# Kernel tuning notes

Measured on AMD Instinct MI355X. Metric: run time of the kernel, lower is better.

## Reference

```python
import jax, jax.numpy as jnp
import numpy as np

BETA = 0.25  # commitment weight (legacy=False)


def setup_inputs() -> dict:
    key = jax.random.key(0)
    k1, k2 = jax.random.split(key)
    B, N_E, E_DIM = 32768, 8192, 256
    z = jax.random.normal(k1, (B, E_DIM), dtype=jnp.float32)
    # embedding initialized uniform(-1/n_e, 1/n_e) as in the torch module
    emb_weight = jax.random.uniform(k2, (N_E, E_DIM), dtype=jnp.float32,
                                    minval=-1.0 / N_E, maxval=1.0 / N_E)
    return {"z": z, "emb_weight": emb_weight}


def reference(z, emb_weight):
    # pairwise squared distances: ||z||^2 + ||e||^2 - 2 z.e   -> [B, n_e]
    d = (jnp.sum(z * z, axis=1, keepdims=True)
         + jnp.sum(emb_weight * emb_weight, axis=1)
         - 2.0 * jnp.einsum('bd,nd->bn', z, emb_weight))
    idx = jnp.argmin(d, axis=1)            # [B]
    z_q = emb_weight[idx]                  # [B, e_dim] gather
    sg = jax.lax.stop_gradient
    loss = (BETA * jnp.mean((sg(z_q) - z) ** 2)
            + jnp.mean((z_q - sg(z)) ** 2))
    z_q_st = z + sg(z_q - z)               # straight-through estimator
    return (z_q_st, loss)
```

## Files before the change

### kernel.cpp

```cpp
#include <hip/hip_runtime.h>
#include <hip/hip_bf16.h>


#define B_ROWS 32768
#define N_E    8192
#define E_DIM  256
#define NSPLIT 4
#define NB     32
#define TILE_B (NB * 256)
#define NBUF   4
#define NIT    ((N_E / NSPLIT) / NB)
#define IDXMASK 0xFFFFE000u

typedef __attribute__((ext_vector_type(4)))  float f32x4;
typedef __attribute__((ext_vector_type(16))) float f32x16;
typedef __attribute__((ext_vector_type(4)))  int   i32x4;
typedef __attribute__((ext_vector_type(8)))  int   i32x8;

#define WAIT_BAR(N) asm volatile("s_waitcnt vmcnt(" #N ")\n\ts_barrier" ::: "memory")

__global__ void cast_e_kernel(const float* __restrict__ emb,
                              int* __restrict__ eb8) {
    int row  = (blockIdx.x * blockDim.x + threadIdx.x) >> 6;
    int lane = threadIdx.x & 63;
    if (row >= N_E) return;
    const float4 v = ((const float4*)(emb + (size_t)row * E_DIM))[lane];
    const float s = 8192.0f;
    int r = __builtin_amdgcn_cvt_pk_fp8_f32(v.x * s, v.y * s, 0, false);
    r     = __builtin_amdgcn_cvt_pk_fp8_f32(v.z * s, v.w * s, r, true);
    eb8[(size_t)row * 64 + lane] = r;
}

__device__ __forceinline__ void stage_tile(char* buf, const char* ebB,
                                           int n0, int wv, int lane) {
    #pragma unroll
    for (int r = 0; r < 2; ++r) {
        const int addr = r * 4096 + (wv * 64 + lane) * 16;
        const int e  = addr >> 8;
        const int Xs = addr & 255;
        const int o  = Xs ^ ((e & 15) << 4);
        const char* src = ebB + ((size_t)(n0 + e) << 8) + o;
        __builtin_amdgcn_global_load_lds((const void*)src,
                                         (void*)(buf + addr), 16, 0, 0);
    }
}

__global__ __launch_bounds__(256, 2) void vq_main_kernel(
        const float* __restrict__ z,
        const int* __restrict__ eb8,
        float* __restrict__ bval) {
    __shared__ __align__(16) char lds[NBUF][TILE_B];
    char* lds0 = &lds[0][0];
    const int tid  = threadIdx.x;
    const int lane = tid & 63;
    const int wv   = tid >> 6;
    const int e    = lane & 31;
    const int hi   = lane >> 5;
    const int rowblk = (int)blockIdx.x >> 2;
    const int split  = (int)blockIdx.x & 3;
    const int rowbase = rowblk * 256 + wv * 64;
    const int n_begin = split * (N_E / NSPLIT);
    const char* ebB = (const char*)eb8;

    i32x8 a[2][4];
    #pragma unroll
    for (int s = 0; s < 2; ++s) {
        const float* zr = z + (size_t)(rowbase + s * 32 + e) * E_DIM + hi * 32;
        #pragma unroll
        for (int c = 0; c < 4; ++c) {
            const float4* p = (const float4*)(zr + c * 64);
            i32x8 f;
            #pragma unroll
            for (int q = 0; q < 8; ++q) {
                const float4 v = p[q];
                int r = __builtin_amdgcn_cvt_pk_fp8_f32(v.x, v.y, 0, false);
                r     = __builtin_amdgcn_cvt_pk_fp8_f32(v.z, v.w, r, true);
                f[q] = r;
            }
            a[s][c] = f;
        }
    }

    int boff[8];
    #pragma unroll
    for (int i = 0; i < 8; ++i) {
        const int X = (i >> 1) * 64 + hi * 32 + (i & 1) * 16;
        boff[i] = e * 256 + (X ^ ((e & 15) << 4));
    }

    float rmax[2][16];
    #pragma unroll
    for (int s = 0; s < 2; ++s)
        #pragma unroll
        for (int r = 0; r < 16; ++r) rmax[s][r] = -__builtin_huge_valf();

    unsigned ibase = (unsigned)(n_begin + e);

    auto compute = [&](int t) {
        const char* cbuf = lds0 + (t & (NBUF - 1)) * TILE_B;
        i32x8 b[4];
        #pragma unroll
        for (int c = 0; c < 4; ++c) {
            const i32x4 lo = *(const i32x4*)(cbuf + boff[c * 2]);
            const i32x4 hi4 = *(const i32x4*)(cbuf + boff[c * 2 + 1]);
            b[c][0] = lo[0]; b[c][1] = lo[1]; b[c][2] = lo[2]; b[c][3] = lo[3];
            b[c][4] = hi4[0]; b[c][5] = hi4[1]; b[c][6] = hi4[2]; b[c][7] = hi4[3];
        }
        f32x16 acc0 = {0.f,0.f,0.f,0.f,0.f,0.f,0.f,0.f,
                       0.f,0.f,0.f,0.f,0.f,0.f,0.f,0.f};
        f32x16 acc1 = acc0;
        __builtin_amdgcn_s_setprio(1);
        #pragma unroll
        for (int c = 0; c < 4; ++c) {
            acc0 = __builtin_amdgcn_mfma_scale_f32_32x32x64_f8f6f4(
                a[0][c], b[c], acc0, 0, 0, 0, 127, 0, 127);
            acc1 = __builtin_amdgcn_mfma_scale_f32_32x32x64_f8f6f4(
                a[1][c], b[c], acc1, 0, 0, 0, 127, 0, 127);
        }
        __builtin_amdgcn_s_setprio(0);
        #pragma unroll
        for (int r = 0; r < 16; ++r) {
            unsigned p0 = (__builtin_bit_cast(unsigned, acc0[r]) & IDXMASK) | ibase;
            rmax[0][r] = fmaxf(rmax[0][r], __builtin_bit_cast(float, p0));
            unsigned p1 = (__builtin_bit_cast(unsigned, acc1[r]) & IDXMASK) | ibase;
            rmax[1][r] = fmaxf(rmax[1][r], __builtin_bit_cast(float, p1));
        }
        ibase += NB;
    };

    stage_tile(lds0 + 0 * TILE_B, ebB, n_begin + 0 * NB, wv, lane);
    stage_tile(lds0 + 1 * TILE_B, ebB, n_begin + 1 * NB, wv, lane);
    stage_tile(lds0 + 2 * TILE_B, ebB, n_begin + 2 * NB, wv, lane);

    #pragma unroll 1
    for (int t = 0; t < NIT - 2; ++t) {
        WAIT_BAR(4);
        if (t < NIT - 3)
            stage_tile(lds0 + ((t + 3) & (NBUF - 1)) * TILE_B, ebB,
                       n_begin + (t + 3) * NB, wv, lane);
        compute(t);
    }
    WAIT_BAR(2);
    compute(NIT - 2);
    WAIT_BAR(0);
    compute(NIT - 1);

    #pragma unroll
    for (int s = 0; s < 2; ++s) {
        #pragma unroll
        for (int r = 0; r < 16; ++r) {
            float v = rmax[s][r];
            #pragma unroll
            for (int bit = 1; bit < 32; bit <<= 1)
                v = fmaxf(v, __shfl_xor(v, bit));
            if (e == 0) {
                const int row = rowbase + s * 32 + (r & 3) + 8 * (r >> 2) + 4 * hi;
                bval[(size_t)split * B_ROWS + row] = v;
            }
        }
    }
}

__global__ void gather_kernel(const float* __restrict__ z,
                              const float* __restrict__ emb,
                              const float* __restrict__ bval,
                              float* __restrict__ out,
                              float* __restrict__ partials) {
    __shared__ float sred[4];
    const int lane   = threadIdx.x & 63;
    const int waveid = threadIdx.x >> 6;
    const int row    = blockIdx.x * 4 + waveid;

    float bv = bval[row];
    #pragma unroll
    for (int s = 1; s < NSPLIT; ++s)
        bv = fmaxf(bv, bval[(size_t)s * B_ROWS + row]);
    const int idx = (int)(__builtin_bit_cast(unsigned, bv) & 0x1FFFu);

    const float4 e  = ((const float4*)(emb + (size_t)idx * E_DIM))[lane];
    const float4 zz = ((const float4*)(z + (size_t)row * E_DIM))[lane];
    ((float4*)(out + (size_t)row * E_DIM))[lane] = e;

    float dx = e.x - zz.x, dy = e.y - zz.y, dz = e.z - zz.z, dw = e.w - zz.w;
    float s = dx * dx + dy * dy + dz * dz + dw * dw;
    #pragma unroll
    for (int off = 32; off; off >>= 1) s += __shfl_xor(s, off);
    if (lane == 0) sred[waveid] = s;
    __syncthreads();
    if (threadIdx.x == 0)
        partials[blockIdx.x] = (sred[0] + sred[1]) + (sred[2] + sred[3]);
}

__global__ void loss_kernel(const float* __restrict__ partials,
                            float* __restrict__ out) {
    __shared__ float sm[256];
    float s = 0.f;
    for (int i = threadIdx.x; i < B_ROWS / 4; i += 256) s += partials[i];
    sm[threadIdx.x] = s;
    __syncthreads();
    for (int off = 128; off; off >>= 1) {
        if (threadIdx.x < off) sm[threadIdx.x] += sm[threadIdx.x + off];
        __syncthreads();
    }
    if (threadIdx.x == 0)
        out[(size_t)B_ROWS * E_DIM] = 1.25f * sm[0] / (float)((size_t)B_ROWS * E_DIM);
}

extern "C" void kernel_launch(void* const* d_in, const int* in_sizes, int n_in,
                              void* d_out, int out_size, void* d_ws, size_t ws_size,
                              hipStream_t stream) {
    const float* z   = (const float*)d_in[0];
    const float* emb = (const float*)d_in[1];
    float* out = (float*)d_out;

    char* ws = (char*)d_ws;
    int*    eb8      = (int*)ws;
    float*  bval     = (float*)(ws + (2u << 20));
    float*  partials = (float*)(ws + (2u << 20) + (512u << 10));

    hipLaunchKernelGGL(cast_e_kernel, dim3(N_E / 4), dim3(256), 0, stream, emb, eb8);
    hipLaunchKernelGGL(vq_main_kernel, dim3(128 * NSPLIT), dim3(256), 0, stream, z, eb8, bval);
    hipLaunchKernelGGL(gather_kernel, dim3(B_ROWS / 4), dim3(256), 0, stream, z, emb, bval, out, partials);
    hipLaunchKernelGGL(loss_kernel, dim3(1), dim3(256), 0, stream, partials, out);
}
```

Baseline: 103.1 us.

## Double-buffer LDS codebook fragments in registers to overlap reads with MFMA

Splits the per-tile work into an LDS-to-register load step and an MFMA/argmax step. The main loop is unrolled by two with ping-pong register buffers, so the next tile's fragments are read from LDS while the current tile's MFMAs run. The global-to-LDS prefetch schedule and wait counts are adjusted to match, with a new epilogue. This hides LDS read latency behind matrix work, at the cost of about 32 extra VGPRs per lane and more complex wait and barrier ordering.

```diff
diff --git a/kernel.cpp b/kernel.cpp
--- a/kernel.cpp
+++ b/kernel.cpp
@@ -96,16 +96,17 @@
 
     unsigned ibase = (unsigned)(n_begin + e);
 
-    auto compute = [&](int t) {
+    auto load_b = [&](i32x8* dst, int t) {
         const char* cbuf = lds0 + (t & (NBUF - 1)) * TILE_B;
-        i32x8 b[4];
         #pragma unroll
         for (int c = 0; c < 4; ++c) {
-            const i32x4 lo = *(const i32x4*)(cbuf + boff[c * 2]);
+            const i32x4 lo  = *(const i32x4*)(cbuf + boff[c * 2]);
             const i32x4 hi4 = *(const i32x4*)(cbuf + boff[c * 2 + 1]);
-            b[c][0] = lo[0]; b[c][1] = lo[1]; b[c][2] = lo[2]; b[c][3] = lo[3];
-            b[c][4] = hi4[0]; b[c][5] = hi4[1]; b[c][6] = hi4[2]; b[c][7] = hi4[3];
-        }
+            dst[c] = __builtin_shufflevector(lo, hi4, 0, 1, 2, 3, 4, 5, 6, 7);
+        }
+    };
+
+    auto mfma_pack = [&](const i32x8* b) {
         f32x16 acc0 = {0.f,0.f,0.f,0.f,0.f,0.f,0.f,0.f,
                        0.f,0.f,0.f,0.f,0.f,0.f,0.f,0.f};
         f32x16 acc1 = acc0;
@@ -128,22 +129,39 @@
         ibase += NB;
     };
 
+    i32x8 bA[4], bB[4];
+
     stage_tile(lds0 + 0 * TILE_B, ebB, n_begin + 0 * NB, wv, lane);
     stage_tile(lds0 + 1 * TILE_B, ebB, n_begin + 1 * NB, wv, lane);
     stage_tile(lds0 + 2 * TILE_B, ebB, n_begin + 2 * NB, wv, lane);
+    WAIT_BAR(4);
+    load_b(bA, 0);
 
     #pragma unroll 1
-    for (int t = 0; t < NIT - 2; ++t) {
-        WAIT_BAR(4);
-        if (t < NIT - 3)
-            stage_tile(lds0 + ((t + 3) & (NBUF - 1)) * TILE_B, ebB,
-                       n_begin + (t + 3) * NB, wv, lane);
-        compute(t);
+    for (int t = 0; t < NIT - 4; t += 2) {
+        WAIT_BAR(2);
+        stage_tile(lds0 + ((t + 3) & (NBUF - 1)) * TILE_B, ebB,
+                   n_begin + (t + 3) * NB, wv, lane);
+        load_b(bB, t + 1);
+        mfma_pack(bA);
+        WAIT_BAR(2);
+        stage_tile(lds0 + ((t + 4) & (NBUF - 1)) * TILE_B, ebB,
+                   n_begin + (t + 4) * NB, wv, lane);
+        load_b(bA, t + 2);
+        mfma_pack(bB);
     }
     WAIT_BAR(2);
-    compute(NIT - 2);
+    stage_tile(lds0 + ((NIT - 1) & (NBUF - 1)) * TILE_B, ebB,
+               n_begin + (NIT - 1) * NB, wv, lane);
+    load_b(bB, NIT - 3);
+    mfma_pack(bA);
+    WAIT_BAR(2);
+    load_b(bA, NIT - 2);
+    mfma_pack(bB);
     WAIT_BAR(0);
-    compute(NIT - 1);
+    load_b(bB, NIT - 1);
+    mfma_pack(bA);
+    mfma_pack(bB);
 
     #pragma unroll
     for (int s = 0; s < 2; ++s) {
```

Measured after the change: 103.4 us. About the same (+0.3%).

## Replace LDS-staged codebook tiles with direct per-wave register double-buffered loads

Applied to the files above, without the earlier changes.

Removes the shared-memory staging of FP8 codebook tiles (global_load_lds with a 4-deep ring and barriers). Each single-wave block now loads its B fragments straight from global memory into registers, double-buffered with ping-pong arrays. The grid changes from 256-thread blocks to 64-thread blocks, so there are four times as many blocks. This drops barrier and LDS overhead, but codebook data is no longer shared across waves, so global/L2 traffic for the codebook goes up about fourfold and load latency is less hidden.

```diff
diff --git a/kernel.cpp b/kernel.cpp
--- a/kernel.cpp
+++ b/kernel.cpp
@@ -7,8 +7,6 @@
 #define E_DIM  256
 #define NSPLIT 4
 #define NB     32
-#define TILE_B (NB * 256)
-#define NBUF   4
 #define NIT    ((N_E / NSPLIT) / NB)
 #define IDXMASK 0xFFFFE000u
 
@@ -16,8 +14,6 @@
 typedef __attribute__((ext_vector_type(16))) float f32x16;
 typedef __attribute__((ext_vector_type(4)))  int   i32x4;
 typedef __attribute__((ext_vector_type(8)))  int   i32x8;
-
-#define WAIT_BAR(N) asm volatile("s_waitcnt vmcnt(" #N ")\n\ts_barrier" ::: "memory")
 
 __global__ void cast_e_kernel(const float* __restrict__ emb,
                               int* __restrict__ eb8) {
@@ -31,36 +27,17 @@
     eb8[(size_t)row * 64 + lane] = r;
 }
 
-__device__ __forceinline__ void stage_tile(char* buf, const char* ebB,
-                                           int n0, int wv, int lane) {
-    #pragma unroll
-    for (int r = 0; r < 2; ++r) {
-        const int addr = r * 4096 + (wv * 64 + lane) * 16;
-        const int e  = addr >> 8;
-        const int Xs = addr & 255;
-        const int o  = Xs ^ ((e & 15) << 4);
-        const char* src = ebB + ((size_t)(n0 + e) << 8) + o;
-        __builtin_amdgcn_global_load_lds((const void*)src,
-                                         (void*)(buf + addr), 16, 0, 0);
-    }
-}
-
-__global__ __launch_bounds__(256, 2) void vq_main_kernel(
+__global__ __launch_bounds__(64) void vq_main_kernel(
         const float* __restrict__ z,
         const int* __restrict__ eb8,
         float* __restrict__ bval) {
-    __shared__ __align__(16) char lds[NBUF][TILE_B];
-    char* lds0 = &lds[0][0];
-    const int tid  = threadIdx.x;
-    const int lane = tid & 63;
-    const int wv   = tid >> 6;
+    const int lane = threadIdx.x & 63;
     const int e    = lane & 31;
     const int hi   = lane >> 5;
     const int rowblk = (int)blockIdx.x >> 2;
     const int split  = (int)blockIdx.x & 3;
-    const int rowbase = rowblk * 256 + wv * 64;
+    const int rowbase = rowblk * 64;
     const int n_begin = split * (N_E / NSPLIT);
-    const char* ebB = (const char*)eb8;
 
     i32x8 a[2][4];
     #pragma unroll
@@ -81,13 +58,6 @@
         }
     }
 
-    int boff[8];
-    #pragma unroll
-    for (int i = 0; i < 8; ++i) {
-        const int X = (i >> 1) * 64 + hi * 32 + (i & 1) * 16;
-        boff[i] = e * 256 + (X ^ ((e & 15) << 4));
-    }
-
     float rmax[2][16];
     #pragma unroll
     for (int s = 0; s < 2; ++s)
@@ -96,16 +66,17 @@
 
     unsigned ibase = (unsigned)(n_begin + e);
 
-    auto compute = [&](int t) {
-        const char* cbuf = lds0 + (t & (NBUF - 1)) * TILE_B;
-        i32x8 b[4];
+    auto load_b = [&](i32x8* dst, int n0) {
+        const int* p = eb8 + ((size_t)(n0 + e) << 6) + hi * 8;
         #pragma unroll
         for (int c = 0; c < 4; ++c) {
-            const i32x4 lo = *(const i32x4*)(cbuf + boff[c * 2]);
-            const i32x4 hi4 = *(const i32x4*)(cbuf + boff[c * 2 + 1]);
-            b[c][0] = lo[0]; b[c][1] = lo[1]; b[c][2] = lo[2]; b[c][3] = lo[3];
-            b[c][4] = hi4[0]; b[c][5] = hi4[1]; b[c][6] = hi4[2]; b[c][7] = hi4[3];
+            const i32x4 lo = *(const i32x4*)(p + c * 16);
+            const i32x4 h4 = *(const i32x4*)(p + c * 16 + 4);
+            dst[c] = __builtin_shufflevector(lo, h4, 0, 1, 2, 3, 4, 5, 6, 7);
         }
+    };
+
+    auto mfma_pack = [&](const i32x8* b) {
         f32x16 acc0 = {0.f,0.f,0.f,0.f,0.f,0.f,0.f,0.f,
                        0.f,0.f,0.f,0.f,0.f,0.f,0.f,0.f};
         f32x16 acc1 = acc0;
@@ -128,22 +99,19 @@
         ibase += NB;
     };
 
-    stage_tile(lds0 + 0 * TILE_B, ebB, n_begin + 0 * NB, wv, lane);
-    stage_tile(lds0 + 1 * TILE_B, ebB, n_begin + 1 * NB, wv, lane);
-    stage_tile(lds0 + 2 * TILE_B, ebB, n_begin + 2 * NB, wv, lane);
+    i32x8 bA[4], bB[4];
+    load_b(bA, n_begin);
 
     #pragma unroll 1
-    for (int t = 0; t < NIT - 2; ++t) {
-        WAIT_BAR(4);
-        if (t < NIT - 3)
-            stage_tile(lds0 + ((t + 3) & (NBUF - 1)) * TILE_B, ebB,
-                       n_begin + (t + 3) * NB, wv, lane);
-        compute(t);
+    for (int t = 0; t < NIT - 2; t += 2) {
+        load_b(bB, n_begin + (t + 1) * NB);
+        mfma_pack(bA);
+        load_b(bA, n_begin + (t + 2) * NB);
+        mfma_pack(bB);
     }
-    WAIT_BAR(2);
-    compute(NIT - 2);
-    WAIT_BAR(0);
-    compute(NIT - 1);
+    load_b(bB, n_begin + (NIT - 1) * NB);
+    mfma_pack(bA);
+    mfma_pack(bB);
 
     #pragma unroll
     for (int s = 0; s < 2; ++s) {
@@ -219,7 +187,7 @@
     float*  partials = (float*)(ws + (2u << 20) + (512u << 10));
 
     hipLaunchKernelGGL(cast_e_kernel, dim3(N_E / 4), dim3(256), 0, stream, emb, eb8);
-    hipLaunchKernelGGL(vq_main_kernel, dim3(128 * NSPLIT), dim3(256), 0, stream, z, eb8, bval);
+    hipLaunchKernelGGL(vq_main_kernel, dim3((B_ROWS / 64) * NSPLIT), dim3(64), 0, stream, z, eb8, bval);
     hipLaunchKernelGGL(gather_kernel, dim3(B_ROWS / 4), dim3(256), 0, stream, z, emb, bval, out, partials);
     hipLaunchKernelGGL(loss_kernel, dim3(1), dim3(256), 0, stream, partials, out);
 }
```

New measurement: 171.9 us. 66.6% more time.
